# Performance work log

Hardware: AMD Instinct MI355X
Metric: run time of the kernel (lower is better)

The kernel has to match this reference:

```python
import jax, jax.numpy as jnp
import numpy as np

H = 64          # HIDDEN_DIM
V = 64          # VOCAB_SIZE
LN_EPS = 1e-5   # torch LayerNorm default
D_EPS = 1e-6    # denom epsilon in delta rule
MEM_SCALE = 1.0 # forward default arg


def setup_inputs() -> dict:
    key = jax.random.key(0)
    ks = jax.random.split(key, 8)
    B, L = 16, 2048
    s = lambda k, shape: (jax.random.normal(k, shape, jnp.float32) * 0.05)
    return {
        "seq": jax.random.randint(ks[0], (B, L), 0, V),
        "embed": s(ks[1], (V, H)),
        "W1": s(ks[2], (H, 2 * H)), "b1": jnp.zeros((2 * H,), jnp.float32),
        "W2": s(ks[3], (2 * H, H)), "b2": jnp.zeros((H,), jnp.float32),
        "gamma": jnp.ones((H,), jnp.float32), "beta": jnp.zeros((H,), jnp.float32),
        "Wr": s(ks[4], (H, H)), "br": jnp.zeros((H,), jnp.float32),
        "Wo": s(ks[5], (H, V)), "bo": jnp.zeros((V,), jnp.float32),
    }


def reference(seq, embed, W1, b1, W2, b2, gamma, beta, Wr, br, Wo, bo):
    h = embed[seq]                                  # (B, L, H)
    ff = jax.nn.relu(h @ W1 + b1) @ W2 + b2         # (B, L, H)
    x = h + ff
    mu = x.mean(-1, keepdims=True)
    var = x.var(-1, keepdims=True)                  # biased, as torch LayerNorm
    h = (x - mu) / jnp.sqrt(var + LN_EPS) * gamma + beta

    B = h.shape[0]
    keys = jnp.swapaxes(h[:, :-1, :], 0, 1)         # (L-1, B, H): all but last token

    def step(M, k):                                  # M: (B, H, H), k: (B, H)
        v_pred = jnp.einsum('bij,bj->bi', M, k)
        denom = (k * k).sum(-1, keepdims=True) + D_EPS
        dv = k - v_pred / denom
        M = M + MEM_SCALE * dv[:, :, None] * k[:, None, :]
        return M, None

    M0 = jnp.zeros((B, H, H), h.dtype)
    M, _ = jax.lax.scan(step, M0, keys)

    q = h[:, -1, :]                                  # last token as query
    ctx = jnp.einsum('bij,bj->bi', M, q)             # (B, H)
    return (ctx @ Wr + br) @ Wo + bo                 # (B, V)
```

## Files before the change

kernel.cpp:

```cpp
#include <hip/hip_runtime.h>

#define HDIM 64
#define LSEQ 2048
#define BATCH 16
#define LN_EPS 1e-5f
#define D_EPS 1e-6f
#define NSEG 32
#define CPS 4

typedef unsigned short u16;
typedef unsigned int   u32;
typedef __attribute__((ext_vector_type(8))) short bf16x8;
typedef __attribute__((ext_vector_type(4))) float f32x4;

__device__ __forceinline__ float bf2f(u16 v) {
    return __uint_as_float(((u32)v) << 16);
}
__device__ __forceinline__ u16 f2bf(float f) {
    u32 u = __float_as_uint(f);
    return (u16)((u + 0x7FFFu + ((u >> 16) & 1u)) >> 16);
}

#define A_W1F  0
#define A_W2F  16384
#define A_ER   32768
#define A_HF   50176
#define H_ROWS 66560
#define H_INVD 75264
#define SMEM_BYTES 75520
#define C_S     0
#define C_V     17408
#define C_BM    34816
#define C_Z     39168
#define C_GM    43520

__global__ __launch_bounds__(256, 2) void fused_pc_kernel(
    const int* __restrict__ seq, const float* __restrict__ embed,
    const float* __restrict__ W1, const float* __restrict__ b1,
    const float* __restrict__ W2, const float* __restrict__ b2,
    const float* __restrict__ gamma, const float* __restrict__ beta,
    u32* __restrict__ PK, u16* __restrict__ q_ws)
{
    __shared__ __align__(16) char smem[SMEM_BYTES];
    const int t = threadIdx.x;
    const int b = blockIdx.x >> 5;
    const int s = blockIdx.x & 31;
    const int tok0 = 1984 - 64 * s;

    u16*   hrows  = (u16*)(smem + H_ROWS);
    float* invd_l = (float*)(smem + H_INVD);

    {
        u16*   sW1f = (u16*)(smem + A_W1F);
        u16*   sW2f = (u16*)(smem + A_W2F);
        float* eR   = (float*)(smem + A_ER);
        u16*   hF   = (u16*)(smem + A_HF);

        {
            const float4* s1 = (const float4*)W1;
#pragma unroll
            for (int q = 0; q < 8; ++q) {
                const int m = t + 256 * q;
                const int k = m >> 5;
                const int o0 = (m & 31) * 4;
                const float4 v = s1[m];
                const float e4[4] = {v.x, v.y, v.z, v.w};
                const int ks = k >> 5, l4 = ((k >> 3) & 3) << 4, i = k & 7;
#pragma unroll
                for (int e = 0; e < 4; ++e) {
                    const int o = o0 + e;
                    sW1f[((ks * 8 + (o >> 4)) * 64 + l4 + (o & 15)) * 8 + i] = f2bf(e4[e]);
                }
            }
            const float4* s2 = (const float4*)W2;
#pragma unroll
            for (int q = 0; q < 8; ++q) {
                const int m = t + 256 * q;
                const int k = m >> 4;
                const int o0 = (m & 15) * 4;
                const float4 v = s2[m];
                const float e4[4] = {v.x, v.y, v.z, v.w};
                const int ks = k >> 5, l4 = ((k >> 3) & 3) << 4, i = k & 7;
#pragma unroll
                for (int e = 0; e < 4; ++e) {
                    const int o = o0 + e;
                    sW2f[((ks * 4 + (o >> 4)) * 64 + l4 + (o & 15)) * 8 + i] = f2bf(e4[e]);
                }
            }
        }
        {
            const int tk = t >> 2, p = t & 3;
            const int v = seq[b * LSEQ + tok0 + tk];
            const float* er = embed + v * HDIM + 16 * p;
#pragma unroll
            for (int q = 0; q < 4; ++q)
                *(float4*)&eR[tk * 68 + 16 * p + 4 * q] = *(const float4*)(er + 4 * q);
        }
        __syncthreads();

        const int lane = t & 63;
        const int w    = t >> 6;
        const int g    = lane >> 4;
        const int c    = lane & 15;

        bf16x8 ea[2];
#pragma unroll
        for (int ks = 0; ks < 2; ++ks) {
            const float* src = &eR[(16 * w + c) * 68 + ks * 32 + g * 8];
            const float4 v0 = *(const float4*)src;
            const float4 v1 = *(const float4*)(src + 4);
            bf16x8 f;
            f[0] = (short)f2bf(v0.x); f[1] = (short)f2bf(v0.y);
            f[2] = (short)f2bf(v0.z); f[3] = (short)f2bf(v0.w);
            f[4] = (short)f2bf(v1.x); f[5] = (short)f2bf(v1.y);
            f[6] = (short)f2bf(v1.z); f[7] = (short)f2bf(v1.w);
            ea[ks] = f;
        }

#pragma unroll
        for (int nt = 0; nt < 8; ++nt) {
            const float bv = b1[16 * nt + c];
            f32x4 acc = {bv, bv, bv, bv};
#pragma unroll
            for (int ks = 0; ks < 2; ++ks) {
                const bf16x8 bf = *(const bf16x8*)&sW1f[((ks * 8 + nt) * 64 + lane) * 8];
                acc = __builtin_amdgcn_mfma_f32_16x16x32_bf16(ea[ks], bf, acc, 0, 0, 0);
            }
            const int o   = 16 * nt + c;
            const int ks2 = o >> 5;
            const int l4  = ((o >> 3) & 3) << 4;
            const int i   = o & 7;
#pragma unroll
            for (int r = 0; r < 4; ++r) {
                const float hv = fmaxf(acc[r], 0.f);
                hF[((w * 4 + ks2) * 64 + l4 + g * 4 + r) * 8 + i] = f2bf(hv);
            }
        }

        bf16x8 ha[4];
#pragma unroll
        for (int ks = 0; ks < 4; ++ks)
            ha[ks] = *(const bf16x8*)&hF[((w * 4 + ks) * 64 + lane) * 8];

        float xf[4][4];
#pragma unroll
        for (int nt = 0; nt < 4; ++nt) {
            const float bv = b2[16 * nt + c];
            f32x4 acc = {bv, bv, bv, bv};
#pragma unroll
            for (int ks = 0; ks < 4; ++ks) {
                const bf16x8 bf = *(const bf16x8*)&sW2f[((ks * 4 + nt) * 64 + lane) * 8];
                acc = __builtin_amdgcn_mfma_f32_16x16x32_bf16(ha[ks], bf, acc, 0, 0, 0);
            }
#pragma unroll
            for (int r = 0; r < 4; ++r)
                xf[nt][r] = acc[r] + eR[(16 * w + g * 4 + r) * 68 + 16 * nt + c];
        }

        float s4[4] = {0, 0, 0, 0}, q4[4] = {0, 0, 0, 0};
#pragma unroll
        for (int nt = 0; nt < 4; ++nt)
#pragma unroll
            for (int r = 0; r < 4; ++r) {
                s4[r] += xf[nt][r];
                q4[r] = fmaf(xf[nt][r], xf[nt][r], q4[r]);
            }
#pragma unroll
        for (int m = 1; m < 16; m <<= 1)
#pragma unroll
            for (int r = 0; r < 4; ++r) {
                s4[r] += __shfl_xor(s4[r], m);
                q4[r] += __shfl_xor(q4[r], m);
            }
        float mu[4], rstd[4];
#pragma unroll
        for (int r = 0; r < 4; ++r) {
            mu[r] = s4[r] * (1.0f / 64.0f);
            const float var = q4[r] * (1.0f / 64.0f) - mu[r] * mu[r];
            rstd[r] = 1.0f / sqrtf(var + LN_EPS);
        }

        float hh[4] = {0, 0, 0, 0};
#pragma unroll
        for (int nt = 0; nt < 4; ++nt) {
            const int o = 16 * nt + c;
            const float gm = gamma[o], bt = beta[o];
#pragma unroll
            for (int r = 0; r < 4; ++r) {
                const float ov = (xf[nt][r] - mu[r]) * rstd[r] * gm + bt;
                const u16 rb = f2bf(ov);
                const float qf = bf2f(rb);
                hh[r] = fmaf(qf, qf, hh[r]);
                hrows[(16 * w + g * 4 + r) * 68 + o] = rb;
                if (s == 0 && w == 3 && g == 3 && r == 3)
                    q_ws[b * 64 + o] = rb;
            }
        }
#pragma unroll
        for (int m = 1; m < 16; m <<= 1)
#pragma unroll
            for (int r = 0; r < 4; ++r) hh[r] += __shfl_xor(hh[r], m);
        if (c == 0) {
#pragma unroll
            for (int r = 0; r < 4; ++r)
                invd_l[16 * w + g * 4 + r] = 1.0f / (hh[r] + D_EPS);
        }
    }
    __syncthreads();

    if (s == 0 && t < 64) hrows[63 * 68 + t] = 0;

    {
        float* S  = (float*)(smem + C_S);
        float* V  = (float*)(smem + C_V);
        float* Bm = (float*)(smem + C_BM);
        float* Z  = (float*)(smem + C_Z);
        float* Gm = (float*)(smem + C_GM);

        for (int idx = t; idx < 64 * 64; idx += 256) {
            const int m = idx >> 6, n = idx & 63;
            S[m * 68 + n] = (m == n) ? 1.0f : 0.0f;
            V[m * 68 + n] = 0.0f;
        }

        for (int cc = 0; cc < CPS; ++cc) {
            const int base = 63 - 16 * cc;
            __syncthreads();

            {
                const int i = t >> 4, j = t & 15;
                if (i > j) {
                    const u16* ra = &hrows[(base - i) * 68];
                    const u16* rb = &hrows[(base - j) * 68];
                    float acc = 0.f;
#pragma unroll
                    for (int m = 0; m < 64; m += 4) {
                        const ushort4 a4 = *(const ushort4*)&ra[m];
                        const ushort4 b4 = *(const ushort4*)&rb[m];
                        acc += bf2f(a4.x) * bf2f(b4.x) + bf2f(a4.y) * bf2f(b4.y)
                             + bf2f(a4.z) * bf2f(b4.z) + bf2f(a4.w) * bf2f(b4.w);
                    }
                    Gm[i * 17 + j] = acc * invd_l[base - j];
                }
            }
            __syncthreads();

            if (t < 64) {
                const int n = t;
                float Breg[16];
#pragma unroll
                for (int i = 0; i < 16; ++i) {
                    float acc = bf2f(hrows[(base - i) * 68 + n]);
#pragma unroll
                    for (int j = 0; j < 16; ++j)
                        if (j < i) acc = fmaf(-Gm[i * 17 + j], Breg[j], acc);
                    Breg[i] = acc;
                    Bm[i * 68 + n] = acc;
                }
            }
            __syncthreads();

            {
                const int i  = t & 15;
                const int n0 = (t >> 4) * 4;
                float4 z = make_float4(0.f, 0.f, 0.f, 0.f);
#pragma unroll
                for (int mq = 0; mq < 16; ++mq) {
                    const float4 bq = *(const float4*)&Bm[i * 68 + mq * 4];
                    const float4 s0 = *(const float4*)&S[(mq * 4 + 0) * 68 + n0];
                    const float4 s1 = *(const float4*)&S[(mq * 4 + 1) * 68 + n0];
                    const float4 s2 = *(const float4*)&S[(mq * 4 + 2) * 68 + n0];
                    const float4 s3 = *(const float4*)&S[(mq * 4 + 3) * 68 + n0];
                    z.x = fmaf(bq.x, s0.x, fmaf(bq.y, s1.x, fmaf(bq.z, s2.x, fmaf(bq.w, s3.x, z.x))));
                    z.y = fmaf(bq.x, s0.y, fmaf(bq.y, s1.y, fmaf(bq.z, s2.y, fmaf(bq.w, s3.y, z.y))));
                    z.z = fmaf(bq.x, s0.z, fmaf(bq.y, s1.z, fmaf(bq.z, s2.z, fmaf(bq.w, s3.z, z.z))));
                    z.w = fmaf(bq.x, s0.w, fmaf(bq.y, s1.w, fmaf(bq.z, s2.w, fmaf(bq.w, s3.w, z.w))));
                }
                *(float4*)&Z[i * 68 + n0] = z;
            }
            __syncthreads();

            {
                const int n0 = (t & 15) * 4;
                const int mh = t >> 4;
                float iv16[16];
#pragma unroll
                for (int q4 = 0; q4 < 4; ++q4) {
                    const float4 v4 = *(const float4*)&invd_l[base - 15 + 4 * q4];
                    iv16[15 - 4 * q4]     = v4.x;
                    iv16[15 - 4 * q4 - 1] = v4.y;
                    iv16[15 - 4 * q4 - 2] = v4.z;
                    iv16[15 - 4 * q4 - 3] = v4.w;
                }
                float4 sacc[4], vacc[4];
#pragma unroll
                for (int p = 0; p < 4; ++p) {
                    sacc[p] = *(float4*)&S[(mh + 16 * p) * 68 + n0];
                    vacc[p] = *(float4*)&V[(mh + 16 * p) * 68 + n0];
                }
#pragma unroll
                for (int j = 0; j < 16; ++j) {
                    const float4 zq = *(const float4*)&Z[j * 68 + n0];
                    const float iv = iv16[j];
                    float4 ztq;
                    ztq.x = zq.x * iv; ztq.y = zq.y * iv;
                    ztq.z = zq.z * iv; ztq.w = zq.w * iv;
                    const u16* kr = &hrows[(base - j) * 68];
                    const float k0 = bf2f(kr[mh]);
                    const float k1 = bf2f(kr[mh + 16]);
                    const float k2 = bf2f(kr[mh + 32]);
                    const float k3 = bf2f(kr[mh + 48]);
                    vacc[0].x = fmaf(k0, zq.x, vacc[0].x); vacc[0].y = fmaf(k0, zq.y, vacc[0].y);
                    vacc[0].z = fmaf(k0, zq.z, vacc[0].z); vacc[0].w = fmaf(k0, zq.w, vacc[0].w);
                    vacc[1].x = fmaf(k1, zq.x, vacc[1].x); vacc[1].y = fmaf(k1, zq.y, vacc[1].y);
                    vacc[1].z = fmaf(k1, zq.z, vacc[1].z); vacc[1].w = fmaf(k1, zq.w, vacc[1].w);
                    vacc[2].x = fmaf(k2, zq.x, vacc[2].x); vacc[2].y = fmaf(k2, zq.y, vacc[2].y);
                    vacc[2].z = fmaf(k2, zq.z, vacc[2].z); vacc[2].w = fmaf(k2, zq.w, vacc[2].w);
                    vacc[3].x = fmaf(k3, zq.x, vacc[3].x); vacc[3].y = fmaf(k3, zq.y, vacc[3].y);
                    vacc[3].z = fmaf(k3, zq.z, vacc[3].z); vacc[3].w = fmaf(k3, zq.w, vacc[3].w);
                    sacc[0].x = fmaf(-k0, ztq.x, sacc[0].x); sacc[0].y = fmaf(-k0, ztq.y, sacc[0].y);
                    sacc[0].z = fmaf(-k0, ztq.z, sacc[0].z); sacc[0].w = fmaf(-k0, ztq.w, sacc[0].w);
                    sacc[1].x = fmaf(-k1, ztq.x, sacc[1].x); sacc[1].y = fmaf(-k1, ztq.y, sacc[1].y);
                    sacc[1].z = fmaf(-k1, ztq.z, sacc[1].z); sacc[1].w = fmaf(-k1, ztq.w, sacc[1].w);
                    sacc[2].x = fmaf(-k2, ztq.x, sacc[2].x); sacc[2].y = fmaf(-k2, ztq.y, sacc[2].y);
                    sacc[2].z = fmaf(-k2, ztq.z, sacc[2].z); sacc[2].w = fmaf(-k2, ztq.w, sacc[2].w);
                    sacc[3].x = fmaf(-k3, ztq.x, sacc[3].x); sacc[3].y = fmaf(-k3, ztq.y, sacc[3].y);
                    sacc[3].z = fmaf(-k3, ztq.z, sacc[3].z); sacc[3].w = fmaf(-k3, ztq.w, sacc[3].w);
                }
#pragma unroll
                for (int p = 0; p < 4; ++p) {
                    *(float4*)&S[(mh + 16 * p) * 68 + n0] = sacc[p];
                    *(float4*)&V[(mh + 16 * p) * 68 + n0] = vacc[p];
                }
            }
        }
        __syncthreads();

        u32* pk = PK + ((size_t)(b * NSEG + s) << 12);
        for (int idx = t; idx < 4096; idx += 256) {
            const int j = idx >> 6, i = idx & 63;
            const u32 sb = ((u32)f2bf(S[i * 68 + j])) << 16;
            const u32 vb = (u32)f2bf(V[i * 68 + j]);
            pk[idx] = sb | vb;
        }
    }
}

__global__ __launch_bounds__(256, 1) void final_kernel(
    const u16* __restrict__ q_ws, const u32* __restrict__ PK,
    const float* __restrict__ Wr, const float* __restrict__ br,
    const float* __restrict__ Wo, const float* __restrict__ bo,
    float* __restrict__ out)
{
    const int b    = blockIdx.x;
    const int t    = threadIdx.x;
    const int lane = t & 63;
    const int p    = t >> 6;

    __shared__ float psum[4][72];
    __shared__ float rl[64];
    __shared__ float cs[64], rs[64];

    rl[lane] = bf2f(q_ws[b * 64 + lane]);

    float ctxp = 0.f;
    u32 cur[16], nxt[16];
    {
        const u32* pk0 = PK + ((size_t)(b * NSEG + 0) << 12);
#pragma unroll
        for (int jj = 0; jj < 16; ++jj)
            cur[jj] = pk0[(p * 16 + jj) * 64 + lane];
    }
    __syncthreads();

    for (int s = 0; s < NSEG; ++s) {
        const int sn = (s + 1 < NSEG) ? s + 1 : s;
        const u32* pkn = PK + ((size_t)(b * NSEG + sn) << 12);
#pragma unroll
        for (int jj = 0; jj < 16; ++jj)
            nxt[jj] = pkn[(p * 16 + jj) * 64 + lane];

        float accr = 0.f;
#pragma unroll
        for (int jj = 0; jj < 16; ++jj) {
            const u32 pv = cur[jj];
            const float Sv = __uint_as_float(pv & 0xFFFF0000u);
            const float Vv = __uint_as_float(pv << 16);
            const float rj = rl[p * 16 + jj];
            accr = fmaf(Sv, rj, accr);
            ctxp = fmaf(Vv, rj, ctxp);
        }
        psum[p][lane] = accr;
        __syncthreads();
        const float rn = (psum[0][lane] + psum[1][lane]) + (psum[2][lane] + psum[3][lane]);
        __syncthreads();
        rl[lane] = rn;

#pragma unroll
        for (int jj = 0; jj < 16; ++jj) cur[jj] = nxt[jj];
    }

    psum[p][lane] = ctxp;
    __syncthreads();
    if (t < 64)
        cs[t] = (psum[0][t] + psum[1][t]) + (psum[2][t] + psum[3][t]);
    __syncthreads();

    float rv = (p == 0) ? br[lane] : 0.f;
#pragma unroll
    for (int i = 0; i < 16; ++i)
        rv = fmaf(cs[p * 16 + i], Wr[(p * 16 + i) * HDIM + lane], rv);
    psum[p][lane] = rv;
    __syncthreads();
    if (t < 64)
        rs[t] = (psum[0][t] + psum[1][t]) + (psum[2][t] + psum[3][t]);
    __syncthreads();

    float ov = (p == 0) ? bo[lane] : 0.f;
#pragma unroll
    for (int i = 0; i < 16; ++i)
        ov = fmaf(rs[p * 16 + i], Wo[(p * 16 + i) * HDIM + lane], ov);
    psum[p][lane] = ov;
    __syncthreads();
    if (t < 64)
        out[(size_t)b * HDIM + t] = (psum[0][t] + psum[1][t]) + (psum[2][t] + psum[3][t]);
}

extern "C" void kernel_launch(void* const* d_in, const int* in_sizes, int n_in,
                              void* d_out, int out_size, void* d_ws, size_t ws_size,
                              hipStream_t stream)
{
    const int*   seq   = (const int*)  d_in[0];
    const float* embed = (const float*)d_in[1];
    const float* W1    = (const float*)d_in[2];
    const float* b1    = (const float*)d_in[3];
    const float* W2    = (const float*)d_in[4];
    const float* b2    = (const float*)d_in[5];
    const float* gamma = (const float*)d_in[6];
    const float* beta  = (const float*)d_in[7];
    const float* Wr    = (const float*)d_in[8];
    const float* br    = (const float*)d_in[9];
    const float* Wo    = (const float*)d_in[10];
    const float* bo    = (const float*)d_in[11];

    u32* pk_ws = (u32*)d_ws;
    u16* q_ws  = (u16*)(pk_ws + (size_t)BATCH * NSEG * 4096);
    float* outp = (float*)d_out;

    hipLaunchKernelGGL(fused_pc_kernel, dim3(BATCH * NSEG), dim3(256), 0, stream,
                       seq, embed, W1, b1, W2, b2, gamma, beta, pk_ws, q_ws);
    hipLaunchKernelGGL(final_kernel, dim3(BATCH), dim3(256), 0, stream,
                       q_ws, pk_ws, Wr, br, Wo, bo, outp);
}
```

Before: 127.9 us.

## Move chunked delta-rule segment composition to MFMA with per-wave column ownership

Rewrites the per-segment chunk loop so each wave owns 16 columns of the S/V transfer matrices and keeps them in MFMA accumulator registers. The Gram matrix, the B·S product and the rank-16 updates now use bf16 MFMA instructions, with hi/lo bf16 splitting to recover near-fp32 accuracy. The block-wide __syncthreads between phases are removed, and each wave redundantly computes the Gram and triangular solve for itself. The query-row zeroing moves into the LayerNorm store. The cost is extra split-precision MFMA work and redundant triangular solves in every wave, with a risk of accuracy loss from the bf16 hi/lo approximation.

```diff
diff --git a/kernel.cpp b/kernel.cpp
--- a/kernel.cpp
+++ b/kernel.cpp
@@ -28,11 +28,13 @@
 #define H_ROWS 66560
 #define H_INVD 75264
 #define SMEM_BYTES 75520
-#define C_S     0
-#define C_V     17408
-#define C_BM    34816
-#define C_Z     39168
-#define C_GM    43520
+#define B_GM 0
+#define B_BH 4352
+#define B_BL 13568
+#define B_SH 22784
+#define B_SL 32000
+#define B_ZN 41216
+#define B_ZV 46336
 
 __global__ __launch_bounds__(256, 2) void fused_pc_kernel(
     const int* __restrict__ seq, const float* __restrict__ embed,
@@ -50,6 +52,11 @@
     u16*   hrows  = (u16*)(smem + H_ROWS);
     float* invd_l = (float*)(smem + H_INVD);
 
+    const int lane = t & 63;
+    const int w    = t >> 6;
+    const int g    = lane >> 4;
+    const int c    = lane & 15;
+
     {
         u16*   sW1f = (u16*)(smem + A_W1F);
         u16*   sW2f = (u16*)(smem + A_W2F);
@@ -97,11 +104,6 @@
                 *(float4*)&eR[tk * 68 + 16 * p + 4 * q] = *(const float4*)(er + 4 * q);
         }
         __syncthreads();
-
-        const int lane = t & 63;
-        const int w    = t >> 6;
-        const int g    = lane >> 4;
-        const int c    = lane & 15;
 
         bf16x8 ea[2];
 #pragma unroll
@@ -191,9 +193,12 @@
                 const u16 rb = f2bf(ov);
                 const float qf = bf2f(rb);
                 hh[r] = fmaf(qf, qf, hh[r]);
-                hrows[(16 * w + g * 4 + r) * 68 + o] = rb;
-                if (s == 0 && w == 3 && g == 3 && r == 3)
+                u16 st = rb;
+                if (s == 0 && w == 3 && g == 3 && r == 3) {
                     q_ws[b * 64 + o] = rb;
+                    st = 0;
+                }
+                hrows[(16 * w + g * 4 + r) * 68 + o] = st;
             }
         }
 #pragma unroll
@@ -208,140 +213,161 @@
     }
     __syncthreads();
 
-    if (s == 0 && t < 64) hrows[63 * 68 + t] = 0;
-
     {
-        float* S  = (float*)(smem + C_S);
-        float* V  = (float*)(smem + C_V);
-        float* Bm = (float*)(smem + C_BM);
-        float* Z  = (float*)(smem + C_Z);
-        float* Gm = (float*)(smem + C_GM);
-
-        for (int idx = t; idx < 64 * 64; idx += 256) {
-            const int m = idx >> 6, n = idx & 63;
-            S[m * 68 + n] = (m == n) ? 1.0f : 0.0f;
-            V[m * 68 + n] = 0.0f;
+        float* Gm = (float*)(smem + B_GM) + w * 272;
+        u16*   Bh = (u16*)(smem + B_BH) + w * 1152;
+        u16*   Bl = (u16*)(smem + B_BL) + w * 1152;
+        u16*   Sh = (u16*)(smem + B_SH) + w * 1152;
+        u16*   Sl = (u16*)(smem + B_SL) + w * 1152;
+        u32*   Zn = (u32*)(smem + B_ZN) + w * 320;
+        u32*   Zv = (u32*)(smem + B_ZV) + w * 320;
+
+        f32x4 Sacc[4], Vacc[4];
+#pragma unroll
+        for (int mt = 0; mt < 4; ++mt) {
+            ushort4 h4, l4;
+            u16* hp = (u16*)&h4;
+#pragma unroll
+            for (int r = 0; r < 4; ++r) {
+                const int m = 16 * mt + 4 * g + r;
+                const float v = (m == 16 * w + c) ? 1.0f : 0.0f;
+                Sacc[mt][r] = v;
+                Vacc[mt][r] = 0.f;
+                hp[r] = f2bf(v);
+            }
+            l4.x = 0; l4.y = 0; l4.z = 0; l4.w = 0;
+            *(ushort4*)&Sh[c * 72 + 16 * mt + 4 * g] = h4;
+            *(ushort4*)&Sl[c * 72 + 16 * mt + 4 * g] = l4;
         }
 
         for (int cc = 0; cc < CPS; ++cc) {
             const int base = 63 - 16 * cc;
-            __syncthreads();
-
+
+            bf16x8 ka[2];
+#pragma unroll
+            for (int f = 0; f < 2; ++f) {
+                const u16* src = &hrows[(base - c) * 68 + f * 32 + g * 8];
+                const ushort4 a0 = *(const ushort4*)src;
+                const ushort4 a1 = *(const ushort4*)(src + 4);
+                bf16x8 kf;
+                kf[0] = (short)a0.x; kf[1] = (short)a0.y; kf[2] = (short)a0.z; kf[3] = (short)a0.w;
+                kf[4] = (short)a1.x; kf[5] = (short)a1.y; kf[6] = (short)a1.z; kf[7] = (short)a1.w;
+                ka[f] = kf;
+            }
+            f32x4 gacc = {0.f, 0.f, 0.f, 0.f};
+            gacc = __builtin_amdgcn_mfma_f32_16x16x32_bf16(ka[0], ka[0], gacc, 0, 0, 0);
+            gacc = __builtin_amdgcn_mfma_f32_16x16x32_bf16(ka[1], ka[1], gacc, 0, 0, 0);
+            const float ivc = invd_l[base - c];
+#pragma unroll
+            for (int r = 0; r < 4; ++r)
+                Gm[(4 * g + r) * 17 + c] = gacc[r] * ivc;
+
+            float Breg[16];
+#pragma unroll
+            for (int i = 0; i < 16; ++i) {
+                float acc = bf2f(hrows[(base - i) * 68 + lane]);
+#pragma unroll
+                for (int j = 0; j < 16; ++j)
+                    if (j < i) acc = fmaf(-Gm[i * 17 + j], Breg[j], acc);
+                Breg[i] = acc;
+            }
+#pragma unroll
+            for (int i = 0; i < 16; ++i) {
+                const u16 hb = f2bf(Breg[i]);
+                const u16 lb = f2bf(Breg[i] - bf2f(hb));
+                Bh[i * 72 + lane] = hb;
+                Bl[i * 72 + lane] = lb;
+            }
+
+            const bf16x8 abh0 = *(const bf16x8*)&Bh[c * 72 +  0 + g * 8];
+            const bf16x8 abh1 = *(const bf16x8*)&Bh[c * 72 + 32 + g * 8];
+            const bf16x8 abl0 = *(const bf16x8*)&Bl[c * 72 +  0 + g * 8];
+            const bf16x8 abl1 = *(const bf16x8*)&Bl[c * 72 + 32 + g * 8];
+            const bf16x8 sh0  = *(const bf16x8*)&Sh[c * 72 +  0 + g * 8];
+            const bf16x8 sh1  = *(const bf16x8*)&Sh[c * 72 + 32 + g * 8];
+            const bf16x8 sl0  = *(const bf16x8*)&Sl[c * 72 +  0 + g * 8];
+            const bf16x8 sl1  = *(const bf16x8*)&Sl[c * 72 + 32 + g * 8];
+            f32x4 zacc = {0.f, 0.f, 0.f, 0.f};
+            zacc = __builtin_amdgcn_mfma_f32_16x16x32_bf16(abh0, sh0, zacc, 0, 0, 0);
+            zacc = __builtin_amdgcn_mfma_f32_16x16x32_bf16(abh1, sh1, zacc, 0, 0, 0);
+            zacc = __builtin_amdgcn_mfma_f32_16x16x32_bf16(abh0, sl0, zacc, 0, 0, 0);
+            zacc = __builtin_amdgcn_mfma_f32_16x16x32_bf16(abh1, sl1, zacc, 0, 0, 0);
+            zacc = __builtin_amdgcn_mfma_f32_16x16x32_bf16(abl0, sh0, zacc, 0, 0, 0);
+            zacc = __builtin_amdgcn_mfma_f32_16x16x32_bf16(abl1, sh1, zacc, 0, 0, 0);
+
+            uint4 znp, zvp;
+            u32* znpp = (u32*)&znp;
+            u32* zvpp = (u32*)&zvp;
+#pragma unroll
+            for (int r = 0; r < 4; ++r) {
+                const int j = 4 * g + r;
+                const float iv = invd_l[base - j];
+                const float z  = zacc[r];
+                const float zt = -z * iv;
+                const u16 nh = f2bf(zt);
+                const u16 nl = f2bf(zt - bf2f(nh));
+                znpp[r] = ((u32)nh << 16) | (u32)nl;
+                const u16 vh = f2bf(z);
+                const u16 vl = f2bf(z - bf2f(vh));
+                zvpp[r] = ((u32)vh << 16) | (u32)vl;
+            }
+            *(uint4*)&Zn[c * 20 + 4 * g] = znp;
+            *(uint4*)&Zv[c * 20 + 4 * g] = zvp;
+
+            const int j0 = (g & 1) * 8;
+            const uint4 za0 = *(const uint4*)&Zn[c * 20 + j0];
+            const uint4 za1 = *(const uint4*)&Zn[c * 20 + j0 + 4];
+            const uint4 zb0 = *(const uint4*)&Zv[c * 20 + j0];
+            const uint4 zb1 = *(const uint4*)&Zv[c * 20 + j0 + 4];
+            bf16x8 znf, zvf;
             {
-                const int i = t >> 4, j = t & 15;
-                if (i > j) {
-                    const u16* ra = &hrows[(base - i) * 68];
-                    const u16* rb = &hrows[(base - j) * 68];
-                    float acc = 0.f;
-#pragma unroll
-                    for (int m = 0; m < 64; m += 4) {
-                        const ushort4 a4 = *(const ushort4*)&ra[m];
-                        const ushort4 b4 = *(const ushort4*)&rb[m];
-                        acc += bf2f(a4.x) * bf2f(b4.x) + bf2f(a4.y) * bf2f(b4.y)
-                             + bf2f(a4.z) * bf2f(b4.z) + bf2f(a4.w) * bf2f(b4.w);
+                const u32 zn8[8] = {za0.x, za0.y, za0.z, za0.w, za1.x, za1.y, za1.z, za1.w};
+                const u32 zv8[8] = {zb0.x, zb0.y, zb0.z, zb0.w, zb1.x, zb1.y, zb1.z, zb1.w};
+                const bool hi = (g < 2);
+#pragma unroll
+                for (int i8 = 0; i8 < 8; ++i8) {
+                    znf[i8] = (short)(hi ? (zn8[i8] >> 16) : (zn8[i8] & 0xFFFFu));
+                    zvf[i8] = (short)(hi ? (zv8[i8] >> 16) : (zv8[i8] & 0xFFFFu));
+                }
+            }
+
+#pragma unroll
+            for (int mt = 0; mt < 4; ++mt) {
+                bf16x8 kaf;
+#pragma unroll
+                for (int i8 = 0; i8 < 8; ++i8)
+                    kaf[i8] = (short)hrows[(base - (j0 + i8)) * 68 + 16 * mt + c];
+                Sacc[mt] = __builtin_amdgcn_mfma_f32_16x16x32_bf16(kaf, znf, Sacc[mt], 0, 0, 0);
+                Vacc[mt] = __builtin_amdgcn_mfma_f32_16x16x32_bf16(kaf, zvf, Vacc[mt], 0, 0, 0);
+            }
+            if (cc < CPS - 1) {
+#pragma unroll
+                for (int mt = 0; mt < 4; ++mt) {
+                    ushort4 h4, l4;
+                    u16* hp = (u16*)&h4;
+                    u16* lp = (u16*)&l4;
+#pragma unroll
+                    for (int r = 0; r < 4; ++r) {
+                        const float sv = Sacc[mt][r];
+                        const u16 hb = f2bf(sv);
+                        hp[r] = hb;
+                        lp[r] = f2bf(sv - bf2f(hb));
                     }
-                    Gm[i * 17 + j] = acc * invd_l[base - j];
+                    *(ushort4*)&Sh[c * 72 + 16 * mt + 4 * g] = h4;
+                    *(ushort4*)&Sl[c * 72 + 16 * mt + 4 * g] = l4;
                 }
             }
-            __syncthreads();
-
-            if (t < 64) {
-                const int n = t;
-                float Breg[16];
-#pragma unroll
-                for (int i = 0; i < 16; ++i) {
-                    float acc = bf2f(hrows[(base - i) * 68 + n]);
-#pragma unroll
-                    for (int j = 0; j < 16; ++j)
-                        if (j < i) acc = fmaf(-Gm[i * 17 + j], Breg[j], acc);
-                    Breg[i] = acc;
-                    Bm[i * 68 + n] = acc;
-                }
-            }
-            __syncthreads();
-
-            {
-                const int i  = t & 15;
-                const int n0 = (t >> 4) * 4;
-                float4 z = make_float4(0.f, 0.f, 0.f, 0.f);
-#pragma unroll
-                for (int mq = 0; mq < 16; ++mq) {
-                    const float4 bq = *(const float4*)&Bm[i * 68 + mq * 4];
-                    const float4 s0 = *(const float4*)&S[(mq * 4 + 0) * 68 + n0];
-                    const float4 s1 = *(const float4*)&S[(mq * 4 + 1) * 68 + n0];
-                    const float4 s2 = *(const float4*)&S[(mq * 4 + 2) * 68 + n0];
-                    const float4 s3 = *(const float4*)&S[(mq * 4 + 3) * 68 + n0];
-                    z.x = fmaf(bq.x, s0.x, fmaf(bq.y, s1.x, fmaf(bq.z, s2.x, fmaf(bq.w, s3.x, z.x))));
-                    z.y = fmaf(bq.x, s0.y, fmaf(bq.y, s1.y, fmaf(bq.z, s2.y, fmaf(bq.w, s3.y, z.y))));
-                    z.z = fmaf(bq.x, s0.z, fmaf(bq.y, s1.z, fmaf(bq.z, s2.z, fmaf(bq.w, s3.z, z.z))));
-                    z.w = fmaf(bq.x, s0.w, fmaf(bq.y, s1.w, fmaf(bq.z, s2.w, fmaf(bq.w, s3.w, z.w))));
-                }
-                *(float4*)&Z[i * 68 + n0] = z;
-            }
-            __syncthreads();
-
-            {
-                const int n0 = (t & 15) * 4;
-                const int mh = t >> 4;
-                float iv16[16];
-#pragma unroll
-                for (int q4 = 0; q4 < 4; ++q4) {
-                    const float4 v4 = *(const float4*)&invd_l[base - 15 + 4 * q4];
-                    iv16[15 - 4 * q4]     = v4.x;
-                    iv16[15 - 4 * q4 - 1] = v4.y;
-                    iv16[15 - 4 * q4 - 2] = v4.z;
-                    iv16[15 - 4 * q4 - 3] = v4.w;
-                }
-                float4 sacc[4], vacc[4];
-#pragma unroll
-                for (int p = 0; p < 4; ++p) {
-                    sacc[p] = *(float4*)&S[(mh + 16 * p) * 68 + n0];
-                    vacc[p] = *(float4*)&V[(mh + 16 * p) * 68 + n0];
-                }
-#pragma unroll
-                for (int j = 0; j < 16; ++j) {
-                    const float4 zq = *(const float4*)&Z[j * 68 + n0];
-                    const float iv = iv16[j];
-                    float4 ztq;
-                    ztq.x = zq.x * iv; ztq.y = zq.y * iv;
-                    ztq.z = zq.z * iv; ztq.w = zq.w * iv;
-                    const u16* kr = &hrows[(base - j) * 68];
-                    const float k0 = bf2f(kr[mh]);
-                    const float k1 = bf2f(kr[mh + 16]);
-                    const float k2 = bf2f(kr[mh + 32]);
-                    const float k3 = bf2f(kr[mh + 48]);
-                    vacc[0].x = fmaf(k0, zq.x, vacc[0].x); vacc[0].y = fmaf(k0, zq.y, vacc[0].y);
-                    vacc[0].z = fmaf(k0, zq.z, vacc[0].z); vacc[0].w = fmaf(k0, zq.w, vacc[0].w);
-                    vacc[1].x = fmaf(k1, zq.x, vacc[1].x); vacc[1].y = fmaf(k1, zq.y, vacc[1].y);
-                    vacc[1].z = fmaf(k1, zq.z, vacc[1].z); vacc[1].w = fmaf(k1, zq.w, vacc[1].w);
-                    vacc[2].x = fmaf(k2, zq.x, vacc[2].x); vacc[2].y = fmaf(k2, zq.y, vacc[2].y);
-                    vacc[2].z = fmaf(k2, zq.z, vacc[2].z); vacc[2].w = fmaf(k2, zq.w, vacc[2].w);
-                    vacc[3].x = fmaf(k3, zq.x, vacc[3].x); vacc[3].y = fmaf(k3, zq.y, vacc[3].y);
-                    vacc[3].z = fmaf(k3, zq.z, vacc[3].z); vacc[3].w = fmaf(k3, zq.w, vacc[3].w);
-                    sacc[0].x = fmaf(-k0, ztq.x, sacc[0].x); sacc[0].y = fmaf(-k0, ztq.y, sacc[0].y);
-                    sacc[0].z = fmaf(-k0, ztq.z, sacc[0].z); sacc[0].w = fmaf(-k0, ztq.w, sacc[0].w);
-                    sacc[1].x = fmaf(-k1, ztq.x, sacc[1].x); sacc[1].y = fmaf(-k1, ztq.y, sacc[1].y);
-                    sacc[1].z = fmaf(-k1, ztq.z, sacc[1].z); sacc[1].w = fmaf(-k1, ztq.w, sacc[1].w);
-                    sacc[2].x = fmaf(-k2, ztq.x, sacc[2].x); sacc[2].y = fmaf(-k2, ztq.y, sacc[2].y);
-                    sacc[2].z = fmaf(-k2, ztq.z, sacc[2].z); sacc[2].w = fmaf(-k2, ztq.w, sacc[2].w);
-                    sacc[3].x = fmaf(-k3, ztq.x, sacc[3].x); sacc[3].y = fmaf(-k3, ztq.y, sacc[3].y);
-                    sacc[3].z = fmaf(-k3, ztq.z, sacc[3].z); sacc[3].w = fmaf(-k3, ztq.w, sacc[3].w);
-                }
-#pragma unroll
-                for (int p = 0; p < 4; ++p) {
-                    *(float4*)&S[(mh + 16 * p) * 68 + n0] = sacc[p];
-                    *(float4*)&V[(mh + 16 * p) * 68 + n0] = vacc[p];
-                }
-            }
-        }
-        __syncthreads();
+        }
 
         u32* pk = PK + ((size_t)(b * NSEG + s) << 12);
-        for (int idx = t; idx < 4096; idx += 256) {
-            const int j = idx >> 6, i = idx & 63;
-            const u32 sb = ((u32)f2bf(S[i * 68 + j])) << 16;
-            const u32 vb = (u32)f2bf(V[i * 68 + j]);
-            pk[idx] = sb | vb;
+#pragma unroll
+        for (int mt = 0; mt < 4; ++mt) {
+            uint4 o;
+            u32* op = (u32*)&o;
+#pragma unroll
+            for (int r = 0; r < 4; ++r)
+                op[r] = ((u32)f2bf(Sacc[mt][r]) << 16) | (u32)f2bf(Vacc[mt][r]);
+            *(uint4*)&pk[(16 * w + c) * 64 + 16 * mt + 4 * g] = o;
         }
     }
 }
```

Result: faster. 119.7 us (-6.4%).
